# Kernel tuning notes

Measured on AMD Instinct MI355X. Metric: run time of the kernel, lower is better.

## Reference

```python
import jax, jax.numpy as jnp
import numpy as np

B, N, D, C, ND = 32, 196, 512, 500, 51  # batch, patches, embed dim, classes, 1+50 descriptions


def _l2norm(x):
    return x / jnp.linalg.norm(x, axis=-1, keepdims=True)


def setup_inputs() -> dict:
    key = jax.random.key(0)
    k1, k2, k3, k4 = jax.random.split(key, 4)
    all_text = _l2norm(jax.random.normal(k3, (ND, C, D), jnp.float32))
    return {
        "image_features": _l2norm(jax.random.normal(k1, (B, D), jnp.float32)),
        "local_image_features": _l2norm(jax.random.normal(k2, (B, N, D), jnp.float32)),
        "all_text_features": all_text,
        "mean_text_features": _l2norm(jnp.mean(all_text, axis=0)),
        "topk": 50,
    }


def reference(image_features, local_image_features, all_text_features, mean_text_features, topk):
    # Faithful translation of get_dense_logits2 (m==1 global-feature axis squeezed out).
    base_logits = image_features @ mean_text_features.T                       # [B, C]
    # w[b,n] = <global image feat b, local patch feat n>
    w = jnp.einsum('bd,bnd->bn', image_features, local_image_features)        # [B, N]
    # v[nd,c]: softmax over descriptions of <mean text c, description nd of class c>
    v = jax.nn.softmax(
        jnp.einsum('cd,ncd->nc', mean_text_features, all_text_features), axis=0)  # [ND, C]
    # sim[b,c,nd,m] = <patch m of image b, description nd of class c>
    sim = jnp.einsum('bmd,ncd->bcnm', local_image_features, all_text_features)    # [B, C, ND, N]
    vals, idx = jax.lax.top_k(sim, topk)                                      # [B, C, ND, k] over patch axis
    sim_top = jnp.swapaxes(vals, 2, 3)                                        # [B, C, k, ND]
    # torch: idx[:, 0, :, 0] -> class 0, description 0, all k indices
    sel = idx[:, 0, 0, :]                                                     # [B, k]
    wg = jax.nn.softmax(jnp.take_along_axis(w, sel, axis=1), axis=-1)         # [B, k]
    # weight[b,c,m,n] = wg[b,m] * v[n,c]
    weight = wg[:, None, :, None] * jnp.swapaxes(v, 0, 1)[None, :, None, :]   # [B, C, k, ND]
    bias_logits = jnp.sum(sim_top * weight, axis=(-2, -1))                    # [B, C]
    return base_logits + bias_logits
```

## Files before the change

kernel.cpp:

```cpp
#include <hip/hip_runtime.h>

#define B_ 32
#define N_ 196
#define D_ 512
#define C_ 500
#define ND_ 51

typedef __attribute__((ext_vector_type(8))) short short8_t;
typedef __attribute__((ext_vector_type(4))) unsigned short us4_t;
typedef __attribute__((ext_vector_type(4))) float f32x4;

typedef const __attribute__((address_space(1))) unsigned int* gas_p;
typedef __attribute__((address_space(3))) unsigned int* las_p;
#define GLDS(gp, lp) __builtin_amdgcn_global_load_lds((gas_p)(gp), (las_p)(lp), 16, 0, 0)

__device__ inline unsigned short f2bf(float f) {
    unsigned u = __float_as_uint(f);
    u += 0x7FFFu + ((u >> 16) & 1u);
    return (unsigned short)(u >> 16);
}

template <int CTRL>
__device__ inline float dpp_mov(float x) {
    return __uint_as_float(__builtin_amdgcn_update_dpp(
        __float_as_uint(x), __float_as_uint(x), CTRL, 0xF, 0xF, true));
}
__device__ inline float rsum64(float v) {
    v += dpp_mov<0x121>(v);
    v += dpp_mov<0x122>(v);
    v += dpp_mov<0x124>(v);
    v += dpp_mov<0x128>(v);
    v += __shfl_xor(v, 16);
    v += __shfl_xor(v, 32);
    return v;
}
__device__ inline float rmax64(float v) {
    v = fmaxf(v, dpp_mov<0x121>(v));
    v = fmaxf(v, dpp_mov<0x122>(v));
    v = fmaxf(v, dpp_mov<0x124>(v));
    v = fmaxf(v, dpp_mov<0x128>(v));
    v = fmaxf(v, __shfl_xor(v, 16));
    v = fmaxf(v, __shfl_xor(v, 32));
    return v;
}
template <int S>
__device__ inline float xsh(float y) {
    if constexpr (S == 1) return dpp_mov<0xB1>(y);
    else if constexpr (S == 2) return dpp_mov<0x4E>(y);
    else if constexpr (S == 8) return dpp_mov<0x128>(y);
    else return __shfl_xor(y, S);
}

__global__ __launch_bounds__(256) void k_cvt(const float4* __restrict__ src,
                                             us4_t* __restrict__ dst, int n4) {
    const int i = blockIdx.x * 256 + threadIdx.x;
    if (i < n4) {
        float4 f = src[i];
        us4_t p = {f2bf(f.x), f2bf(f.y), f2bf(f.z), f2bf(f.w)};
        dst[i] = p;
    }
}

__global__ __launch_bounds__(256) void k_v(const float* __restrict__ mean,
                                           const float* __restrict__ text,
                                           float* __restrict__ vout) {
    const int c = blockIdx.x;
    const int w = threadIdx.x >> 6, lane = threadIdx.x & 63;
    __shared__ float sc[ND_];
    float md[8];
#pragma unroll
    for (int t = 0; t < 8; ++t) md[t] = mean[c * 512 + lane + 64 * t];
    for (int j = 0; j < 13; ++j) {
        const int n = w + 4 * j;
        if (n < ND_) {
            const float* tp = &text[((size_t)n * C_ + c) * 512];
            float a = 0.f;
#pragma unroll
            for (int t = 0; t < 8; ++t) a += md[t] * tp[lane + 64 * t];
            a = rsum64(a);
            if (lane == 0) sc[n] = a;
        }
    }
    __syncthreads();
    if (w == 0) {
        float xv = (lane < ND_) ? sc[lane] : -INFINITY;
        float mx = rmax64(xv);
        float e = (lane < ND_) ? expf(xv - mx) : 0.f;
        float sum = rsum64(e);
        if (lane < ND_) vout[lane * C_ + c] = e / sum;
    }
}

__global__ __launch_bounds__(256) void k_sw(const float* __restrict__ image,
                                            const float* __restrict__ localf,
                                            const float* __restrict__ text,
                                            float* __restrict__ s_ws,
                                            float* __restrict__ wm_ws) {
    const int b = blockIdx.x;
    const int m0 = blockIdx.y * 28;
    const int w = threadIdx.x >> 6, lane = threadIdx.x & 63;
    float t00[8], img[8];
#pragma unroll
    for (int t = 0; t < 8; ++t) {
        t00[t] = text[lane + 64 * t];
        img[t] = image[b * 512 + lane + 64 * t];
    }
    for (int t7 = 0; t7 < 7; ++t7) {
        const int m = m0 + w * 7 + t7;
        const float* lp = &localf[((size_t)b * N_ + m) * 512];
        float a = 0.f, g = 0.f;
#pragma unroll
        for (int t = 0; t < 8; ++t) {
            const float lv = lp[lane + 64 * t];
            a += t00[t] * lv;
            g += img[t] * lv;
        }
        a = rsum64(a);
        g = rsum64(g);
        if (lane == 0) { s_ws[b * N_ + m] = a; wm_ws[b * N_ + m] = g; }
    }
}

__global__ __launch_bounds__(64) void k_sel(const float* __restrict__ s_ws,
                                            const float* __restrict__ wm_ws,
                                            float* __restrict__ wgout) {
    const int b = blockIdx.x;
    const int lane = threadIdx.x;
    const unsigned long long ltmask = (1ull << lane) - 1ull;
    __shared__ float cv[64], cw[64];

    float x[4], p[4];
#pragma unroll
    for (int i = 0; i < 4; ++i) {
        const int m = lane + 64 * i;
        x[i] = (m < N_) ? s_ws[b * N_ + m] : -INFINITY;
        p[i] = (m < N_) ? wm_ws[b * N_ + m] : 0.f;
    }
    float lo = -1.02f, hi = 1.02f;
    int cl = N_;
    for (int it = 0; it < 24; ++it) {
        const float t = 0.5f * (lo + hi);
        int cnum = 0;
#pragma unroll
        for (int i = 0; i < 4; ++i) cnum += __popcll(__ballot(x[i] > t));
        if (cnum >= 50) { lo = t; cl = cnum; if (cnum <= 64) break; }
        else hi = t;
    }
    bool f[4];
    if (cl <= 64) {
#pragma unroll
        for (int i = 0; i < 4; ++i) f[i] = x[i] > lo;
    } else {
        int s1 = 0;
#pragma unroll
        for (int i = 0; i < 4; ++i) s1 += __popcll(__ballot(x[i] > hi));
        const int need = 64 - s1;
        int run = 0;
#pragma unroll
        for (int i = 0; i < 4; ++i) {
            const bool mid = (x[i] > lo) && !(x[i] > hi);
            const unsigned long long bm = __ballot(mid);
            const int pos = run + __popcll(bm & ltmask);
            f[i] = (x[i] > hi) || (mid && pos < need);
            run += __popcll(bm);
        }
    }
    int basep = 0;
#pragma unroll
    for (int i = 0; i < 4; ++i) {
        const unsigned long long bm = __ballot(f[i]);
        const int pos = basep + __popcll(bm & ltmask);
        if (f[i]) { cv[pos] = x[i]; cw[pos] = p[i]; }
        basep += __popcll(bm);
    }
    __builtin_amdgcn_s_waitcnt(0);
    float y = (lane < basep) ? cv[lane] : -INFINITY;
    float z = (lane < basep) ? cw[lane] : 0.f;
#pragma unroll
    for (int k = 2; k <= 64; k <<= 1) {
#pragma unroll
        for (int s2 = k >> 1; s2 > 0; s2 >>= 1) {
            const float py = __shfl_xor(y, s2);
            const float pz = __shfl_xor(z, s2);
            const bool keep_max = ((lane & k) == 0) == ((lane & s2) == 0);
            const bool take = keep_max ? (py > y) : (py < y);
            if (take) { y = py; z = pz; }
        }
    }
    float xv = (lane < 50) ? z : -INFINITY;
    float mx = xv;
#pragma unroll
    for (int off = 32; off; off >>= 1) mx = fmaxf(mx, __shfl_xor(mx, off));
    float e = (lane < 50) ? expf(xv - mx) : 0.f;
    float sum = e;
#pragma unroll
    for (int off = 32; off; off >>= 1) sum += __shfl_xor(sum, off);
    if (lane < 50) wgout[b * 50 + lane] = e / sum;
}

#define BSTEP(S, UP) { \
    const float q1 = xsh<S>(y1); \
    const float q2 = xsh<S>(y2); \
    if ((q1 > y1) == (UP)) y1 = q1; \
    if ((q2 > y2) == (UP)) y2 = q2; }

__global__ __launch_bounds__(512, 8) void k_main(const float* __restrict__ image,
                                                 const float* __restrict__ mean,
                                                 const unsigned short* __restrict__ localbf,
                                                 const unsigned short* __restrict__ textbf,
                                                 const float* __restrict__ vws,
                                                 const float* __restrict__ wgws,
                                                 float* __restrict__ out) {
    const int b = blockIdx.x;
    const int c = blockIdx.y;
    const int tid = threadIdx.x;
    const int w = tid >> 6;
    const int lane = tid & 63;
    const int quad = lane >> 4;
    const int l16 = lane & 15;

    __shared__ __align__(16) union SU {
        unsigned short stg[ND_ * 196 * 2];
        float ST[ND_ * 196];
    } u;

    float base_reg = 0.f;
    if (w == 0) {
        float s = 0.f;
#pragma unroll
        for (int t = 0; t < 8; ++t)
            s += image[b * 512 + lane + 64 * t] * mean[c * 512 + lane + 64 * t];
        s = rsum64(s);
        base_reg = s;
    }

    f32x4 acc[2][4];
    const f32x4 zv = {0.f, 0.f, 0.f, 0.f};
#pragma unroll
    for (int i = 0; i < 2; ++i)
#pragma unroll
        for (int j = 0; j < 4; ++j) acc[i][j] = zv;

    const unsigned short* abase = localbf + (size_t)(b * N_) * 512;

    for (int ks = 0; ks < 8; ++ks) {
#pragma unroll
        for (int i = 0; i < 4; ++i) {
            const int s = i * 512 + tid;
            if (s < 1568) {
                const int r = s >> 3;
                const int c8 = (s & 7) ^ (r & 7);
                GLDS(abase + (size_t)r * 512 + ks * 64 + c8 * 8, (char*)u.stg + s * 16);
            }
        }
        {
            const int s = tid;
            if (s < 408) {
                const int r = s >> 3;
                const int c8 = (s & 7) ^ (r & 7);
                GLDS(textbf + (size_t)(r * C_ + c) * 512 + ks * 64 + c8 * 8,
                     (char*)u.stg + 25088 + s * 16);
            }
        }
        __syncthreads();
#pragma unroll
        for (int kc = 0; kc < 2; ++kc) {
            short8_t bfr[4];
#pragma unroll
            for (int nt = 0; nt < 4; ++nt) {
                const int row = nt * 16 + l16;
                const int j = kc * 4 + quad;
                bfr[nt] = *(const short8_t*)&u.stg[12544 + row * 64 + ((j ^ (row & 7)) * 8)];
            }
#pragma unroll
            for (int mi = 0; mi < 2; ++mi) {
                const int mt = w + 8 * mi;
                if (mt < 13) {
                    const int row = mt * 16 + l16;
                    const int j = kc * 4 + quad;
                    short8_t af = *(const short8_t*)&u.stg[row * 64 + ((j ^ (row & 7)) * 8)];
#pragma unroll
                    for (int nt = 0; nt < 4; ++nt)
                        acc[mi][nt] = __builtin_amdgcn_mfma_f32_16x16x32_bf16(af, bfr[nt], acc[mi][nt], 0, 0, 0);
                }
            }
        }
        __syncthreads();
    }

#pragma unroll
    for (int nt = 0; nt < 4; ++nt) {
        const int n = nt * 16 + l16;
        if (n < ND_) {
#pragma unroll
            for (int mi = 0; mi < 2; ++mi) {
                const int mt = w + 8 * mi;
                if (mt < 12 || (mt == 12 && quad == 0))
                    *(f32x4*)&u.ST[n * 196 + mt * 16 + quad * 4] = acc[mi][nt];
            }
        }
    }
    __syncthreads();

    const float wgv = (lane < 50) ? wgws[b * 50 + lane] : 0.f;
    const unsigned long long ltmask = (1ull << lane) - 1ull;
    float waveacc = 0.f;

    const bool L0 = (lane & 1) == 0, L1 = (lane & 2) == 0, L2 = (lane & 4) == 0,
               L3 = (lane & 8) == 0, L4 = (lane & 16) == 0, L5 = (lane & 32) == 0;

    for (int t = 0; t < 4; ++t) {
        const int n1 = w + 16 * t;
        const int n2 = n1 + 8;
        const bool a2 = (n2 < ND_);
        if (n1 >= ND_) break;
        float* rowp1 = &u.ST[n1 * 196];
        float* rowp2 = &u.ST[(a2 ? n2 : n1) * 196];

        float x1[4], x2[4];
        if (lane < 49) {
            f32x4 v1 = *(const f32x4*)&rowp1[lane * 4];
            f32x4 v2 = *(const f32x4*)&rowp2[lane * 4];
#pragma unroll
            for (int r = 0; r < 4; ++r) { x1[r] = v1[r]; x2[r] = a2 ? v2[r] : -INFINITY; }
        } else {
#pragma unroll
            for (int r = 0; r < 4; ++r) { x1[r] = -INFINITY; x2[r] = -INFINITY; }
        }

        float lo1 = -1.02f, hi1 = 1.02f, lo2 = -1.02f, hi2 = 1.02f;
        int cl1 = 256, cl2 = a2 ? 256 : 0;
        bool d1 = false, d2 = !a2;
        for (int it = 0; it < 24 && !(d1 && d2); ++it) {
            const float t1 = 0.5f * (lo1 + hi1);
            const float t2 = 0.5f * (lo2 + hi2);
            int c1 = 0, c2 = 0;
#pragma unroll
            for (int i = 0; i < 4; ++i) {
                c1 += __popcll(__ballot(x1[i] > t1));
                c2 += __popcll(__ballot(x2[i] > t2));
            }
            if (!d1) { if (c1 >= 50) { lo1 = t1; cl1 = c1; d1 = (c1 <= 64); } else hi1 = t1; }
            if (!d2) { if (c2 >= 50) { lo2 = t2; cl2 = c2; d2 = (c2 <= 64); } else hi2 = t2; }
        }

        bool f1[4], f2[4];
        int cnt1, cnt2;
        if (cl1 <= 64) {
#pragma unroll
            for (int i = 0; i < 4; ++i) f1[i] = x1[i] > lo1;
            cnt1 = cl1;
        } else {
            int s1 = 0;
#pragma unroll
            for (int i = 0; i < 4; ++i) s1 += __popcll(__ballot(x1[i] > hi1));
            const int need = 64 - s1;
            int run = 0;
#pragma unroll
            for (int i = 0; i < 4; ++i) {
                const bool mid = (x1[i] > lo1) && !(x1[i] > hi1);
                const unsigned long long bm = __ballot(mid);
                const int pos = run + __popcll(bm & ltmask);
                f1[i] = (x1[i] > hi1) || (mid && pos < need);
                run += __popcll(bm);
            }
            cnt1 = 64;
        }
        if (cl2 <= 64) {
#pragma unroll
            for (int i = 0; i < 4; ++i) f2[i] = x2[i] > lo2;
            cnt2 = cl2;
        } else {
            int s1 = 0;
#pragma unroll
            for (int i = 0; i < 4; ++i) s1 += __popcll(__ballot(x2[i] > hi2));
            const int need = 64 - s1;
            int run = 0;
#pragma unroll
            for (int i = 0; i < 4; ++i) {
                const bool mid = (x2[i] > lo2) && !(x2[i] > hi2);
                const unsigned long long bm = __ballot(mid);
                const int pos = run + __popcll(bm & ltmask);
                f2[i] = (x2[i] > hi2) || (mid && pos < need);
                run += __popcll(bm);
            }
            cnt2 = 64;
        }

        int bp1 = 0, bp2 = 0;
#pragma unroll
        for (int i = 0; i < 4; ++i) {
            const unsigned long long bm1 = __ballot(f1[i]);
            const unsigned long long bm2 = __ballot(f2[i]);
            const int p1 = bp1 + __popcll(bm1 & ltmask);
            const int p2 = bp2 + __popcll(bm2 & ltmask);
            if (f1[i]) rowp1[p1] = x1[i];
            if (f2[i]) rowp2[p2] = x2[i];
            bp1 += __popcll(bm1);
            bp2 += __popcll(bm2);
        }
        __builtin_amdgcn_s_waitcnt(0);
        float y1 = (lane < cnt1) ? rowp1[lane] : -INFINITY;
        float y2 = (lane < cnt2) ? rowp2[lane] : -INFINITY;

        BSTEP(1, L1 == L0)
        BSTEP(2, L2 == L1) BSTEP(1, L2 == L0)
        BSTEP(4, L3 == L2) BSTEP(2, L3 == L1) BSTEP(1, L3 == L0)
        BSTEP(8, L4 == L3) BSTEP(4, L4 == L2) BSTEP(2, L4 == L1) BSTEP(1, L4 == L0)
        BSTEP(16, L5 == L4) BSTEP(8, L5 == L3) BSTEP(4, L5 == L2) BSTEP(2, L5 == L1) BSTEP(1, L5 == L0)
        BSTEP(32, L5) BSTEP(16, L4) BSTEP(8, L3) BSTEP(4, L2) BSTEP(2, L1) BSTEP(1, L0)

        float part1 = (lane < 50) ? y1 * wgv : 0.f;
        float part2 = (lane < 50) ? y2 * wgv : 0.f;
        part1 = rsum64(part1);
        part2 = rsum64(part2);
        waveacc += vws[n1 * C_ + c] * part1;
        if (a2) waveacc += vws[n2 * C_ + c] * part2;
    }

    if (lane == 0) u.ST[w * 196] = waveacc;
    __syncthreads();
    if (tid == 0) {
        float r = base_reg;
#pragma unroll
        for (int i = 0; i < 8; ++i) r += u.ST[i * 196];
        out[b * C_ + c] = r;
    }
}

__global__ __launch_bounds__(256) void k_main_fb(const float* __restrict__ image,
                                                 const float* __restrict__ localf,
                                                 const float* __restrict__ text,
                                                 const float* __restrict__ mean,
                                                 const float* __restrict__ vws,
                                                 const float* __restrict__ wgws,
                                                 float* __restrict__ out) {
    const int c = blockIdx.x;
    const int b = blockIdx.y;
    const int tid = threadIdx.x;
    const int w = tid >> 6;
    const int lane = tid & 63;
    const int quad = lane >> 4;
    const int l16 = lane & 15;

    __shared__ __align__(16) union SU {
        struct { unsigned short A[208 * 72]; unsigned short Bm[64 * 72]; } st;
        float S[208 * 65];
    } u;
    __shared__ float wavepart[4];
    __shared__ float basev;

    if (w == 0) {
        float s = 0.f;
#pragma unroll
        for (int t = 0; t < 8; ++t)
            s += image[b * 512 + lane + 64 * t] * mean[c * 512 + lane + 64 * t];
#pragma unroll
        for (int off = 32; off; off >>= 1) s += __shfl_xor(s, off);
        if (lane == 0) basev = s;
    }

    f32x4 acc[4][4];
    const f32x4 zv = {0.f, 0.f, 0.f, 0.f};
#pragma unroll
    for (int i = 0; i < 4; ++i)
#pragma unroll
        for (int j = 0; j < 4; ++j) acc[i][j] = zv;

    const int lbase = (b * N_) * 512;
    for (int ks = 0; ks < 8; ++ks) {
        const int k0 = ks * 64;
        for (int e = tid; e < 3328; e += 256) {
            const int m = e >> 4, kc4 = e & 15;
            float4 fv = make_float4(0.f, 0.f, 0.f, 0.f);
            if (m < N_) fv = *(const float4*)&localf[lbase + m * 512 + k0 + kc4 * 4];
            us4_t pk = {f2bf(fv.x), f2bf(fv.y), f2bf(fv.z), f2bf(fv.w)};
            *(us4_t*)&u.st.A[m * 72 + kc4 * 4] = pk;
        }
        for (int e = tid; e < 1024; e += 256) {
            const int n = e >> 4, kc4 = e & 15;
            float4 fv = make_float4(0.f, 0.f, 0.f, 0.f);
            if (n < ND_) fv = *(const float4*)&text[((size_t)n * C_ + c) * 512 + k0 + kc4 * 4];
            us4_t pk = {f2bf(fv.x), f2bf(fv.y), f2bf(fv.z), f2bf(fv.w)};
            *(us4_t*)&u.st.Bm[n * 72 + kc4 * 4] = pk;
        }
        __syncthreads();
#pragma unroll
        for (int kc = 0; kc < 2; ++kc) {
            short8_t bfr[4];
#pragma unroll
            for (int nt = 0; nt < 4; ++nt)
                bfr[nt] = *(const short8_t*)&u.st.Bm[(nt * 16 + l16) * 72 + kc * 32 + quad * 8];
#pragma unroll
            for (int mi = 0; mi < 4; ++mi) {
                const int mt = w + 4 * mi;
                if (mt < 13) {
                    short8_t af = *(const short8_t*)&u.st.A[(mt * 16 + l16) * 72 + kc * 32 + quad * 8];
#pragma unroll
                    for (int nt = 0; nt < 4; ++nt)
                        acc[mi][nt] = __builtin_amdgcn_mfma_f32_16x16x32_bf16(af, bfr[nt], acc[mi][nt], 0, 0, 0);
                }
            }
        }
        __syncthreads();
    }

#pragma unroll
    for (int mi = 0; mi < 4; ++mi) {
        const int mt = w + 4 * mi;
        if (mt < 13) {
#pragma unroll
            for (int nt = 0; nt < 4; ++nt)
#pragma unroll
                for (int r = 0; r < 4; ++r)
                    u.S[(mt * 16 + quad * 4 + r) * 65 + nt * 16 + l16] = acc[mi][nt][r];
        }
    }
    __syncthreads();

    const float wgv = (lane < 50) ? wgws[b * 50 + lane] : 0.f;
    float waveacc = 0.f;

    for (int j = 0; j < 13; ++j) {
        const int n = w + 4 * j;
        if (n < ND_) {
            float x[4];
#pragma unroll
            for (int i = 0; i < 4; ++i) {
                const int m = lane + 64 * i;
                x[i] = (m < N_) ? u.S[m * 65 + n] : -INFINITY;
            }
#pragma unroll
            for (int k = 2; k <= 64; k <<= 1) {
#pragma unroll
                for (int s2 = k >> 1; s2 > 0; s2 >>= 1) {
                    const bool up = ((lane & k) == 0) == ((lane & s2) == 0);
#pragma unroll
                    for (int r = 0; r < 4; ++r) {
                        const float p = __shfl_xor(x[r], s2);
                        x[r] = up ? fmaxf(x[r], p) : fminf(x[r], p);
                    }
                }
            }
            float m01 = fmaxf(x[0], __shfl_xor(x[1], 63));
            float m23 = fmaxf(x[2], __shfl_xor(x[3], 63));
#pragma unroll
            for (int s2 = 32; s2 > 0; s2 >>= 1) {
                const bool up = (lane & s2) == 0;
                const float p0 = __shfl_xor(m01, s2);
                const float p1 = __shfl_xor(m23, s2);
                m01 = up ? fmaxf(m01, p0) : fminf(m01, p0);
                m23 = up ? fmaxf(m23, p1) : fminf(m23, p1);
            }
            float y = fmaxf(m01, __shfl_xor(m23, 63));
#pragma unroll
            for (int s2 = 32; s2 > 0; s2 >>= 1) {
                const bool up = (lane & s2) == 0;
                const float p = __shfl_xor(y, s2);
                y = up ? fmaxf(y, p) : fminf(y, p);
            }
            float part = (lane < 50) ? y * wgv : 0.f;
#pragma unroll
            for (int off = 32; off; off >>= 1) part += __shfl_xor(part, off);
            waveacc += vws[n * C_ + c] * part;
        }
    }

    if (lane == 0) wavepart[w] = waveacc;
    __syncthreads();
    if (tid == 0)
        out[b * C_ + c] = basev + wavepart[0] + wavepart[1] + wavepart[2] + wavepart[3];
}

extern "C" void kernel_launch(void* const* d_in, const int* in_sizes, int n_in,
                              void* d_out, int out_size, void* d_ws, size_t ws_size,
                              hipStream_t stream) {
    (void)in_sizes; (void)n_in; (void)out_size;
    const float* image = (const float*)d_in[0];
    const float* localf = (const float*)d_in[1];
    const float* text  = (const float*)d_in[2];
    const float* mean  = (const float*)d_in[3];
    float* out = (float*)d_out;

    float* vws   = (float*)d_ws;
    float* wgws  = vws + ND_ * C_;
    float* s_ws  = wgws + B_ * 50;
    float* wm_ws = s_ws + B_ * N_;
    const size_t small_bytes = (size_t)(ND_ * C_ + B_ * 50 + 2 * B_ * N_) * 4;
    const size_t bf_bytes = ((size_t)B_ * N_ * D_ + (size_t)ND_ * C_ * D_) * 2;

    hipLaunchKernelGGL(k_v, dim3(C_), dim3(256), 0, stream, mean, text, vws);
    hipLaunchKernelGGL(k_sw, dim3(B_, 7), dim3(256), 0, stream, image, localf, text, s_ws, wm_ws);
    hipLaunchKernelGGL(k_sel, dim3(B_), dim3(64), 0, stream, s_ws, wm_ws, wgws);

    if (ws_size >= small_bytes + bf_bytes) {
        unsigned short* localbf = (unsigned short*)(wm_ws + B_ * N_);
        unsigned short* textbf  = localbf + (size_t)B_ * N_ * D_;
        const int n4_local = B_ * N_ * D_ / 4;
        const int n4_text  = ND_ * C_ * D_ / 4;
        hipLaunchKernelGGL(k_cvt, dim3((n4_local + 255) / 256), dim3(256), 0, stream,
                           (const float4*)localf, (us4_t*)localbf, n4_local);
        hipLaunchKernelGGL(k_cvt, dim3((n4_text + 255) / 256), dim3(256), 0, stream,
                           (const float4*)text, (us4_t*)textbf, n4_text);
        hipLaunchKernelGGL(k_main, dim3(B_, C_), dim3(512), 0, stream,
                           image, mean, localbf, textbf, vws, wgws, out);
    } else {
        hipLaunchKernelGGL(k_main_fb, dim3(C_, B_), dim3(256), 0, stream,
                           image, localf, text, mean, vws, wgws, out);
    }
}
```

Before: 679.1 us.

## Fuse bf16 conversion with dot-product prepasses and use integer-key top-k selection

The standalone bf16 conversion kernels are merged into the kernels that already read the same fp32 data. The text conversion now also computes the mean-text dot products, followed by a small per-class softmax kernel. The local-feature conversion also computes the class-0 similarity and global-weight dot products. This removes repeated full reads of the large text and local tensors. In the main kernel, top-k selection switches from float bisection over a fixed range to order-preserving unsigned keys, bisecting from the actual row maximum. That is meant to converge in fewer iterations, at the cost of extra key conversion and a wave max reduction.

```diff
diff --git a/kernel.cpp b/kernel.cpp
--- a/kernel.cpp
+++ b/kernel.cpp
@@ -20,10 +20,22 @@
     return (unsigned short)(u >> 16);
 }
 
+__device__ inline unsigned f2key(float f) {
+    const unsigned u = __float_as_uint(f);
+    return u ^ ((unsigned)((int)u >> 31) | 0x80000000u);
+}
+__device__ inline float key2f(unsigned k) {
+    return __uint_as_float(k ^ (~(unsigned)((int)k >> 31) | 0x80000000u));
+}
+
 template <int CTRL>
 __device__ inline float dpp_mov(float x) {
     return __uint_as_float(__builtin_amdgcn_update_dpp(
         __float_as_uint(x), __float_as_uint(x), CTRL, 0xF, 0xF, true));
+}
+template <int CTRL>
+__device__ inline unsigned dpp_movu(unsigned x) {
+    return (unsigned)__builtin_amdgcn_update_dpp((int)x, (int)x, CTRL, 0xF, 0xF, true);
 }
 __device__ inline float rsum64(float v) {
     v += dpp_mov<0x121>(v);
@@ -43,22 +55,86 @@
     v = fmaxf(v, __shfl_xor(v, 32));
     return v;
 }
+__device__ inline unsigned rumax64(unsigned v) {
+    unsigned t;
+    t = dpp_movu<0x121>(v); v = (t > v) ? t : v;
+    t = dpp_movu<0x122>(v); v = (t > v) ? t : v;
+    t = dpp_movu<0x124>(v); v = (t > v) ? t : v;
+    t = dpp_movu<0x128>(v); v = (t > v) ? t : v;
+    t = (unsigned)__shfl_xor((int)v, 16); v = (t > v) ? t : v;
+    t = (unsigned)__shfl_xor((int)v, 32); v = (t > v) ? t : v;
+    return v;
+}
 template <int S>
-__device__ inline float xsh(float y) {
-    if constexpr (S == 1) return dpp_mov<0xB1>(y);
-    else if constexpr (S == 2) return dpp_mov<0x4E>(y);
-    else if constexpr (S == 8) return dpp_mov<0x128>(y);
-    else return __shfl_xor(y, S);
-}
-
-__global__ __launch_bounds__(256) void k_cvt(const float4* __restrict__ src,
-                                             us4_t* __restrict__ dst, int n4) {
-    const int i = blockIdx.x * 256 + threadIdx.x;
-    if (i < n4) {
-        float4 f = src[i];
-        us4_t p = {f2bf(f.x), f2bf(f.y), f2bf(f.z), f2bf(f.w)};
-        dst[i] = p;
-    }
+__device__ inline unsigned xshu(unsigned y) {
+    if constexpr (S == 1) return dpp_movu<0xB1>(y);
+    else if constexpr (S == 2) return dpp_movu<0x4E>(y);
+    else if constexpr (S == 8) return dpp_movu<0x128>(y);
+    else return (unsigned)__shfl_xor((int)y, S);
+}
+
+__global__ __launch_bounds__(256) void k_ctd(const float* __restrict__ text,
+                                             const float* __restrict__ mean,
+                                             unsigned short* __restrict__ textbf,
+                                             float* __restrict__ dots) {
+    const int row = blockIdx.x * 4 + (threadIdx.x >> 6);
+    const int lane = threadIdx.x & 63;
+    const int n = row / C_;
+    const int ccol = row - n * C_;
+    const float* tp = text + (size_t)row * 512 + lane * 8;
+    const float* mp = mean + (size_t)ccol * 512 + lane * 8;
+    const float4 f0 = *(const float4*)tp;
+    const float4 f1 = *(const float4*)(tp + 4);
+    const float4 m0 = *(const float4*)mp;
+    const float4 m1 = *(const float4*)(mp + 4);
+    float a = f0.x * m0.x + f0.y * m0.y + f0.z * m0.z + f0.w * m0.w
+            + f1.x * m1.x + f1.y * m1.y + f1.z * m1.z + f1.w * m1.w;
+    a = rsum64(a);
+    const us4_t p0 = {f2bf(f0.x), f2bf(f0.y), f2bf(f0.z), f2bf(f0.w)};
+    const us4_t p1 = {f2bf(f1.x), f2bf(f1.y), f2bf(f1.z), f2bf(f1.w)};
+    *(us4_t*)&textbf[(size_t)row * 512 + lane * 8] = p0;
+    *(us4_t*)&textbf[(size_t)row * 512 + lane * 8 + 4] = p1;
+    if (lane == 0) dots[row] = a;
+}
+
+__global__ __launch_bounds__(64) void k_vsm(const float* __restrict__ dots,
+                                            float* __restrict__ vout) {
+    const int ccol = blockIdx.x * 64 + threadIdx.x;
+    if (ccol >= C_) return;
+    float mx = -INFINITY;
+    for (int n = 0; n < ND_; ++n) mx = fmaxf(mx, dots[n * C_ + ccol]);
+    float sum = 0.f;
+    for (int n = 0; n < ND_; ++n) sum += expf(dots[n * C_ + ccol] - mx);
+    for (int n = 0; n < ND_; ++n) vout[n * C_ + ccol] = expf(dots[n * C_ + ccol] - mx) / sum;
+}
+
+__global__ __launch_bounds__(256) void k_cls(const float* __restrict__ image,
+                                             const float* __restrict__ localf,
+                                             const float* __restrict__ text,
+                                             unsigned short* __restrict__ localbf,
+                                             float* __restrict__ s_ws,
+                                             float* __restrict__ wm_ws) {
+    const int row = blockIdx.x * 4 + (threadIdx.x >> 6);
+    const int lane = threadIdx.x & 63;
+    const int b = row / N_;
+    const float* lp = localf + (size_t)row * 512 + lane * 8;
+    const float4 l0 = *(const float4*)lp;
+    const float4 l1 = *(const float4*)(lp + 4);
+    const float* ip = image + b * 512 + lane * 8;
+    const float* t0p = text + lane * 8;
+    const float4 i0 = *(const float4*)ip, i1 = *(const float4*)(ip + 4);
+    const float4 t0 = *(const float4*)t0p, t1 = *(const float4*)(t0p + 4);
+    float a = l0.x * t0.x + l0.y * t0.y + l0.z * t0.z + l0.w * t0.w
+            + l1.x * t1.x + l1.y * t1.y + l1.z * t1.z + l1.w * t1.w;
+    float g = l0.x * i0.x + l0.y * i0.y + l0.z * i0.z + l0.w * i0.w
+            + l1.x * i1.x + l1.y * i1.y + l1.z * i1.z + l1.w * i1.w;
+    a = rsum64(a);
+    g = rsum64(g);
+    const us4_t p0 = {f2bf(l0.x), f2bf(l0.y), f2bf(l0.z), f2bf(l0.w)};
+    const us4_t p1 = {f2bf(l1.x), f2bf(l1.y), f2bf(l1.z), f2bf(l1.w)};
+    *(us4_t*)&localbf[(size_t)row * 512 + lane * 8] = p0;
+    *(us4_t*)&localbf[(size_t)row * 512 + lane * 8 + 4] = p1;
+    if (lane == 0) { s_ws[row] = a; wm_ws[row] = g; }
 }
 
 __global__ __launch_bounds__(256) void k_v(const float* __restrict__ mean,
@@ -198,9 +274,9 @@
     if (lane < 50) wgout[b * 50 + lane] = e / sum;
 }
 
-#define BSTEP(S, UP) { \
-    const float q1 = xsh<S>(y1); \
-    const float q2 = xsh<S>(y2); \
+#define BSTEPU(S, UP) { \
+    const unsigned q1 = xshu<S>(y1); \
+    const unsigned q2 = xshu<S>(y2); \
     if ((q1 > y1) == (UP)) y1 = q1; \
     if ((q2 > y2) == (UP)) y2 = q2; }
 
@@ -316,29 +392,43 @@
         if (n1 >= ND_) break;
         float* rowp1 = &u.ST[n1 * 196];
         float* rowp2 = &u.ST[(a2 ? n2 : n1) * 196];
-
-        float x1[4], x2[4];
+        unsigned* rp1 = (unsigned*)rowp1;
+        unsigned* rp2 = (unsigned*)rowp2;
+
+        unsigned k1[4], k2[4];
         if (lane < 49) {
-            f32x4 v1 = *(const f32x4*)&rowp1[lane * 4];
-            f32x4 v2 = *(const f32x4*)&rowp2[lane * 4];
-#pragma unroll
-            for (int r = 0; r < 4; ++r) { x1[r] = v1[r]; x2[r] = a2 ? v2[r] : -INFINITY; }
+            const f32x4 v1 = *(const f32x4*)&rowp1[lane * 4];
+            const f32x4 v2 = *(const f32x4*)&rowp2[lane * 4];
+#pragma unroll
+            for (int r = 0; r < 4; ++r) {
+                k1[r] = f2key(v1[r]);
+                k2[r] = a2 ? f2key(v2[r]) : 0u;
+            }
         } else {
 #pragma unroll
-            for (int r = 0; r < 4; ++r) { x1[r] = -INFINITY; x2[r] = -INFINITY; }
-        }
-
-        float lo1 = -1.02f, hi1 = 1.02f, lo2 = -1.02f, hi2 = 1.02f;
+            for (int r = 0; r < 4; ++r) { k1[r] = 0u; k2[r] = 0u; }
+        }
+
+        unsigned mx1 = k1[0], mx2 = k2[0];
+#pragma unroll
+        for (int r = 1; r < 4; ++r) {
+            mx1 = (k1[r] > mx1) ? k1[r] : mx1;
+            mx2 = (k2[r] > mx2) ? k2[r] : mx2;
+        }
+        mx1 = rumax64(mx1);
+        mx2 = rumax64(mx2);
+
+        unsigned lo1 = 0u, hi1 = mx1, lo2 = 0u, hi2 = mx2;
         int cl1 = 256, cl2 = a2 ? 256 : 0;
         bool d1 = false, d2 = !a2;
         for (int it = 0; it < 24 && !(d1 && d2); ++it) {
-            const float t1 = 0.5f * (lo1 + hi1);
-            const float t2 = 0.5f * (lo2 + hi2);
+            const unsigned t1 = lo1 + ((hi1 - lo1) >> 1);
+            const unsigned t2 = lo2 + ((hi2 - lo2) >> 1);
             int c1 = 0, c2 = 0;
 #pragma unroll
             for (int i = 0; i < 4; ++i) {
-                c1 += __popcll(__ballot(x1[i] > t1));
-                c2 += __popcll(__ballot(x2[i] > t2));
+                c1 += __popcll(__ballot(k1[i] > t1));
+                c2 += __popcll(__ballot(k2[i] > t2));
             }
             if (!d1) { if (c1 >= 50) { lo1 = t1; cl1 = c1; d1 = (c1 <= 64); } else hi1 = t1; }
             if (!d2) { if (c2 >= 50) { lo2 = t2; cl2 = c2; d2 = (c2 <= 64); } else hi2 = t2; }
@@ -348,40 +438,40 @@
         int cnt1, cnt2;
         if (cl1 <= 64) {
 #pragma unroll
-            for (int i = 0; i < 4; ++i) f1[i] = x1[i] > lo1;
+            for (int i = 0; i < 4; ++i) f1[i] = k1[i] > lo1;
             cnt1 = cl1;
         } else {
             int s1 = 0;
 #pragma unroll
-            for (int i = 0; i < 4; ++i) s1 += __popcll(__ballot(x1[i] > hi1));
+            for (int i = 0; i < 4; ++i) s1 += __popcll(__ballot(k1[i] > hi1));
             const int need = 64 - s1;
             int run = 0;
 #pragma unroll
             for (int i = 0; i < 4; ++i) {
-                const bool mid = (x1[i] > lo1) && !(x1[i] > hi1);
+                const bool mid = (k1[i] > lo1) && !(k1[i] > hi1);
                 const unsigned long long bm = __ballot(mid);
                 const int pos = run + __popcll(bm & ltmask);
-                f1[i] = (x1[i] > hi1) || (mid && pos < need);
+                f1[i] = (k1[i] > hi1) || (mid && pos < need);
                 run += __popcll(bm);
             }
             cnt1 = 64;
         }
         if (cl2 <= 64) {
 #pragma unroll
-            for (int i = 0; i < 4; ++i) f2[i] = x2[i] > lo2;
+            for (int i = 0; i < 4; ++i) f2[i] = k2[i] > lo2;
             cnt2 = cl2;
         } else {
             int s1 = 0;
 #pragma unroll
-            for (int i = 0; i < 4; ++i) s1 += __popcll(__ballot(x2[i] > hi2));
+            for (int i = 0; i < 4; ++i) s1 += __popcll(__ballot(k2[i] > hi2));
             const int need = 64 - s1;
             int run = 0;
 #pragma unroll
             for (int i = 0; i < 4; ++i) {
-                const bool mid = (x2[i] > lo2) && !(x2[i] > hi2);
+                const bool mid = (k2[i] > lo2) && !(k2[i] > hi2);
                 const unsigned long long bm = __ballot(mid);
                 const int pos = run + __popcll(bm & ltmask);
-                f2[i] = (x2[i] > hi2) || (mid && pos < need);
+                f2[i] = (k2[i] > hi2) || (mid && pos < need);
                 run += __popcll(bm);
             }
             cnt2 = 64;
@@ -394,24 +484,26 @@
             const unsigned long long bm2 = __ballot(f2[i]);
             const int p1 = bp1 + __popcll(bm1 & ltmask);
             const int p2 = bp2 + __popcll(bm2 & ltmask);
-            if (f1[i]) rowp1[p1] = x1[i];
-            if (f2[i]) rowp2[p2] = x2[i];
+            if (f1[i]) rp1[p1] = k1[i];
+            if (f2[i]) rp2[p2] = k2[i];
             bp1 += __popcll(bm1);
             bp2 += __popcll(bm2);
         }
         __builtin_amdgcn_s_waitcnt(0);
-        float y1 = (lane < cnt1) ? rowp1[lane] : -INFINITY;
-        float y2 = (lane < cnt2) ? rowp2[lane] : -INFINITY;
-
-        BSTEP(1, L1 == L0)
-        BSTEP(2, L2 == L1) BSTEP(1, L2 == L0)
-        BSTEP(4, L3 == L2) BSTEP(2, L3 == L1) BSTEP(1, L3 == L0)
-        BSTEP(8, L4 == L3) BSTEP(4, L4 == L2) BSTEP(2, L4 == L1) BSTEP(1, L4 == L0)
-        BSTEP(16, L5 == L4) BSTEP(8, L5 == L3) BSTEP(4, L5 == L2) BSTEP(2, L5 == L1) BSTEP(1, L5 == L0)
-        BSTEP(32, L5) BSTEP(16, L4) BSTEP(8, L3) BSTEP(4, L2) BSTEP(2, L1) BSTEP(1, L0)
-
-        float part1 = (lane < 50) ? y1 * wgv : 0.f;
-        float part2 = (lane < 50) ? y2 * wgv : 0.f;
+        unsigned y1 = (lane < cnt1) ? rp1[lane] : 0u;
+        unsigned y2 = (lane < cnt2) ? rp2[lane] : 0u;
+
+        BSTEPU(1, L1 == L0)
+        BSTEPU(2, L2 == L1) BSTEPU(1, L2 == L0)
+        BSTEPU(4, L3 == L2) BSTEPU(2, L3 == L1) BSTEPU(1, L3 == L0)
+        BSTEPU(8, L4 == L3) BSTEPU(4, L4 == L2) BSTEPU(2, L4 == L1) BSTEPU(1, L4 == L0)
+        BSTEPU(16, L5 == L4) BSTEPU(8, L5 == L3) BSTEPU(4, L5 == L2) BSTEPU(2, L5 == L1) BSTEPU(1, L5 == L0)
+        BSTEPU(32, L5) BSTEPU(16, L4) BSTEPU(8, L3) BSTEPU(4, L2) BSTEPU(2, L1) BSTEPU(1, L0)
+
+        const float fy1 = key2f(y1);
+        const float fy2 = key2f(y2);
+        float part1 = (lane < 50) ? fy1 * wgv : 0.f;
+        float part2 = (lane < 50) ? fy2 * wgv : 0.f;
         part1 = rsum64(part1);
         part2 = rsum64(part2);
         waveacc += vws[n1 * C_ + c] * part1;
@@ -586,25 +678,25 @@
     float* wgws  = vws + ND_ * C_;
     float* s_ws  = wgws + B_ * 50;
     float* wm_ws = s_ws + B_ * N_;
-    const size_t small_bytes = (size_t)(ND_ * C_ + B_ * 50 + 2 * B_ * N_) * 4;
+    float* dots  = wm_ws + B_ * N_;
+    const size_t small_bytes = (size_t)(2 * ND_ * C_ + B_ * 50 + 2 * B_ * N_) * 4;
     const size_t bf_bytes = ((size_t)B_ * N_ * D_ + (size_t)ND_ * C_ * D_) * 2;
 
-    hipLaunchKernelGGL(k_v, dim3(C_), dim3(256), 0, stream, mean, text, vws);
-    hipLaunchKernelGGL(k_sw, dim3(B_, 7), dim3(256), 0, stream, image, localf, text, s_ws, wm_ws);
-    hipLaunchKernelGGL(k_sel, dim3(B_), dim3(64), 0, stream, s_ws, wm_ws, wgws);
-
     if (ws_size >= small_bytes + bf_bytes) {
-        unsigned short* localbf = (unsigned short*)(wm_ws + B_ * N_);
+        unsigned short* localbf = (unsigned short*)(dots + ND_ * C_);
         unsigned short* textbf  = localbf + (size_t)B_ * N_ * D_;
-        const int n4_local = B_ * N_ * D_ / 4;
-        const int n4_text  = ND_ * C_ * D_ / 4;
-        hipLaunchKernelGGL(k_cvt, dim3((n4_local + 255) / 256), dim3(256), 0, stream,
-                           (const float4*)localf, (us4_t*)localbf, n4_local);
-        hipLaunchKernelGGL(k_cvt, dim3((n4_text + 255) / 256), dim3(256), 0, stream,
-                           (const float4*)text, (us4_t*)textbf, n4_text);
+        hipLaunchKernelGGL(k_ctd, dim3(ND_ * C_ / 4), dim3(256), 0, stream,
+                           text, mean, textbf, dots);
+        hipLaunchKernelGGL(k_vsm, dim3((C_ + 63) / 64), dim3(64), 0, stream, dots, vws);
+        hipLaunchKernelGGL(k_cls, dim3(B_ * N_ / 4), dim3(256), 0, stream,
+                           image, localf, text, localbf, s_ws, wm_ws);
+        hipLaunchKernelGGL(k_sel, dim3(B_), dim3(64), 0, stream, s_ws, wm_ws, wgws);
         hipLaunchKernelGGL(k_main, dim3(B_, C_), dim3(512), 0, stream,
                            image, mean, localbf, textbf, vws, wgws, out);
     } else {
+        hipLaunchKernelGGL(k_v, dim3(C_), dim3(256), 0, stream, mean, text, vws);
+        hipLaunchKernelGGL(k_sw, dim3(B_, 7), dim3(256), 0, stream, image, localf, text, s_ws, wm_ws);
+        hipLaunchKernelGGL(k_sel, dim3(B_), dim3(64), 0, stream, s_ws, wm_ws, wgws);
         hipLaunchKernelGGL(k_main_fb, dim3(C_, B_), dim3(256), 0, stream,
                            image, localf, text, mean, vws, wgws, out);
     }
```

New measurement: 726.5 us. 7.0% more time.

## Fuse bf16 conversion with softmax-weight and selector dot products in prep kernels

Applied to the files above, without the earlier changes.

Replaces the separate fp32-to-bf16 conversion kernels and the k_v/k_sw preprocessing with fused kernels. These read text and local features once, compute the needed dot products (mean-text dots, class-0 description scores, global-local weights) and write the bf16 copies in the same pass. A small kernel then applies the softmax over descriptions. This removes redundant full reads of the large text tensor. The main kernel's launch-bounds occupancy hint also drops from 8 to 6, trading occupancy for more registers per thread.

```diff
diff --git a/kernel.cpp b/kernel.cpp
--- a/kernel.cpp
+++ b/kernel.cpp
@@ -51,14 +51,68 @@
     else return __shfl_xor(y, S);
 }
 
-__global__ __launch_bounds__(256) void k_cvt(const float4* __restrict__ src,
-                                             us4_t* __restrict__ dst, int n4) {
-    const int i = blockIdx.x * 256 + threadIdx.x;
-    if (i < n4) {
-        float4 f = src[i];
-        us4_t p = {f2bf(f.x), f2bf(f.y), f2bf(f.z), f2bf(f.w)};
-        dst[i] = p;
-    }
+__global__ __launch_bounds__(256) void k_ctd(const float* __restrict__ text,
+                                             const float* __restrict__ mean,
+                                             unsigned short* __restrict__ textbf,
+                                             float* __restrict__ dots) {
+    const int row = blockIdx.x * 4 + (threadIdx.x >> 6);
+    const int lane = threadIdx.x & 63;
+    const int n = row / C_;
+    const int ccol = row - n * C_;
+    const float* tp = text + (size_t)row * 512 + lane * 8;
+    const float* mp = mean + (size_t)ccol * 512 + lane * 8;
+    const float4 f0 = *(const float4*)tp;
+    const float4 f1 = *(const float4*)(tp + 4);
+    const float4 m0 = *(const float4*)mp;
+    const float4 m1 = *(const float4*)(mp + 4);
+    float a = f0.x * m0.x + f0.y * m0.y + f0.z * m0.z + f0.w * m0.w
+            + f1.x * m1.x + f1.y * m1.y + f1.z * m1.z + f1.w * m1.w;
+    a = rsum64(a);
+    const us4_t p0 = {f2bf(f0.x), f2bf(f0.y), f2bf(f0.z), f2bf(f0.w)};
+    const us4_t p1 = {f2bf(f1.x), f2bf(f1.y), f2bf(f1.z), f2bf(f1.w)};
+    *(us4_t*)&textbf[(size_t)row * 512 + lane * 8] = p0;
+    *(us4_t*)&textbf[(size_t)row * 512 + lane * 8 + 4] = p1;
+    if (lane == 0) dots[row] = a;
+}
+
+__global__ __launch_bounds__(64) void k_vsm(const float* __restrict__ dots,
+                                            float* __restrict__ vout) {
+    const int c = blockIdx.x;
+    const int lane = threadIdx.x;
+    float xv = (lane < ND_) ? dots[lane * C_ + c] : -INFINITY;
+    float mx = rmax64(xv);
+    float e = (lane < ND_) ? expf(xv - mx) : 0.f;
+    float sum = rsum64(e);
+    if (lane < ND_) vout[lane * C_ + c] = e / sum;
+}
+
+__global__ __launch_bounds__(256) void k_cls(const float* __restrict__ image,
+                                             const float* __restrict__ localf,
+                                             const float* __restrict__ text,
+                                             unsigned short* __restrict__ localbf,
+                                             float* __restrict__ s_ws,
+                                             float* __restrict__ wm_ws) {
+    const int row = blockIdx.x * 4 + (threadIdx.x >> 6);
+    const int lane = threadIdx.x & 63;
+    const int b = row / N_;
+    const float* lp = localf + (size_t)row * 512 + lane * 8;
+    const float4 l0 = *(const float4*)lp;
+    const float4 l1 = *(const float4*)(lp + 4);
+    const float* ip = image + b * 512 + lane * 8;
+    const float* t0p = text + lane * 8;
+    const float4 i0 = *(const float4*)ip, i1 = *(const float4*)(ip + 4);
+    const float4 t0 = *(const float4*)t0p, t1 = *(const float4*)(t0p + 4);
+    float a = l0.x * t0.x + l0.y * t0.y + l0.z * t0.z + l0.w * t0.w
+            + l1.x * t1.x + l1.y * t1.y + l1.z * t1.z + l1.w * t1.w;
+    float g = l0.x * i0.x + l0.y * i0.y + l0.z * i0.z + l0.w * i0.w
+            + l1.x * i1.x + l1.y * i1.y + l1.z * i1.z + l1.w * i1.w;
+    a = rsum64(a);
+    g = rsum64(g);
+    const us4_t p0 = {f2bf(l0.x), f2bf(l0.y), f2bf(l0.z), f2bf(l0.w)};
+    const us4_t p1 = {f2bf(l1.x), f2bf(l1.y), f2bf(l1.z), f2bf(l1.w)};
+    *(us4_t*)&localbf[(size_t)row * 512 + lane * 8] = p0;
+    *(us4_t*)&localbf[(size_t)row * 512 + lane * 8 + 4] = p1;
+    if (lane == 0) { s_ws[row] = a; wm_ws[row] = g; }
 }
 
 __global__ __launch_bounds__(256) void k_v(const float* __restrict__ mean,
@@ -204,7 +258,7 @@
     if ((q1 > y1) == (UP)) y1 = q1; \
     if ((q2 > y2) == (UP)) y2 = q2; }
 
-__global__ __launch_bounds__(512, 8) void k_main(const float* __restrict__ image,
+__global__ __launch_bounds__(512, 6) void k_main(const float* __restrict__ image,
                                                  const float* __restrict__ mean,
                                                  const unsigned short* __restrict__ localbf,
                                                  const unsigned short* __restrict__ textbf,
@@ -586,25 +640,25 @@
     float* wgws  = vws + ND_ * C_;
     float* s_ws  = wgws + B_ * 50;
     float* wm_ws = s_ws + B_ * N_;
-    const size_t small_bytes = (size_t)(ND_ * C_ + B_ * 50 + 2 * B_ * N_) * 4;
+    float* dots  = wm_ws + B_ * N_;
+    const size_t small_bytes = (size_t)(2 * ND_ * C_ + B_ * 50 + 2 * B_ * N_) * 4;
     const size_t bf_bytes = ((size_t)B_ * N_ * D_ + (size_t)ND_ * C_ * D_) * 2;
 
-    hipLaunchKernelGGL(k_v, dim3(C_), dim3(256), 0, stream, mean, text, vws);
-    hipLaunchKernelGGL(k_sw, dim3(B_, 7), dim3(256), 0, stream, image, localf, text, s_ws, wm_ws);
-    hipLaunchKernelGGL(k_sel, dim3(B_), dim3(64), 0, stream, s_ws, wm_ws, wgws);
-
     if (ws_size >= small_bytes + bf_bytes) {
-        unsigned short* localbf = (unsigned short*)(wm_ws + B_ * N_);
+        unsigned short* localbf = (unsigned short*)(dots + ND_ * C_);
         unsigned short* textbf  = localbf + (size_t)B_ * N_ * D_;
-        const int n4_local = B_ * N_ * D_ / 4;
-        const int n4_text  = ND_ * C_ * D_ / 4;
-        hipLaunchKernelGGL(k_cvt, dim3((n4_local + 255) / 256), dim3(256), 0, stream,
-                           (const float4*)localf, (us4_t*)localbf, n4_local);
-        hipLaunchKernelGGL(k_cvt, dim3((n4_text + 255) / 256), dim3(256), 0, stream,
-                           (const float4*)text, (us4_t*)textbf, n4_text);
+        hipLaunchKernelGGL(k_ctd, dim3(ND_ * C_ / 4), dim3(256), 0, stream,
+                           text, mean, textbf, dots);
+        hipLaunchKernelGGL(k_vsm, dim3(C_), dim3(64), 0, stream, dots, vws);
+        hipLaunchKernelGGL(k_cls, dim3(B_ * N_ / 4), dim3(256), 0, stream,
+                           image, localf, text, localbf, s_ws, wm_ws);
+        hipLaunchKernelGGL(k_sel, dim3(B_), dim3(64), 0, stream, s_ws, wm_ws, wgws);
         hipLaunchKernelGGL(k_main, dim3(B_, C_), dim3(512), 0, stream,
                            image, mean, localbf, textbf, vws, wgws, out);
     } else {
+        hipLaunchKernelGGL(k_v, dim3(C_), dim3(256), 0, stream, mean, text, vws);
+        hipLaunchKernelGGL(k_sw, dim3(B_, 7), dim3(256), 0, stream, image, localf, text, s_ws, wm_ws);
+        hipLaunchKernelGGL(k_sel, dim3(B_), dim3(64), 0, stream, s_ws, wm_ws, wgws);
         hipLaunchKernelGGL(k_main_fb, dim3(C_, B_), dim3(256), 0, stream,
                            image, localf, text, mean, vws, wgws, out);
     }
```

Result: faster. 638.6 us (-6.0%).
